# Optimization experiments

Measured on AMD Instinct MI355X. Metric: run time of the kernel, lower is better.

Reference implementation:

```python
import jax, jax.numpy as jnp
import numpy as np

DIM, H, D, B, L = 1024, 8, 64, 1, 256


def silu(v):
    return v * jax.nn.sigmoid(v)


def setup_inputs() -> dict:
    key = jax.random.key(0)
    ks = jax.random.split(key, 12)
    n = lambda i, shape, scale=1.0: jax.random.normal(ks[i], shape, dtype=jnp.float32) * scale
    return {
        "x": n(0, (B, L, DIM)),
        "hidden_real": n(1, (B, H, D)),
        "hidden_imag": n(2, (B, H, D)),
        "w_in1": n(3, (DIM, DIM), 1.0 / np.sqrt(DIM)),
        "b_in1": jnp.zeros((DIM,), jnp.float32),
        "w_in2": n(4, (DIM, H * D * 4), 1.0 / np.sqrt(DIM)),
        "b_in2": jnp.zeros((H * D * 4,), jnp.float32),
        "w_out1": n(5, (H * D * 2, DIM), 1.0 / np.sqrt(H * D * 2)),
        "b_out1": jnp.zeros((DIM,), jnp.float32),
        "w_out2": n(6, (DIM, DIM), 1.0 / np.sqrt(DIM)),
        "b_out2": jnp.zeros((DIM,), jnp.float32),
        "mat_v_real": n(7, (H, D, D)),
        "mat_v_imag": n(8, (H, D, D)),
    }


def reference(x, hidden_real, hidden_imag, w_in1, b_in1, w_in2, b_in2,
              w_out1, b_out1, w_out2, b_out2, mat_v_real, mat_v_imag):
    batch, slen, _ = x.shape
    t = silu(x @ w_in1 + b_in1)
    t = t @ w_in2 + b_in2                       # (B, L, 4*H*D)
    z = t.reshape(batch, slen, H, D, 2, 2)      # [..., {x,a}, {re,im}]
    xc = jax.lax.complex(z[..., 0, 0], z[..., 0, 1])   # (B, L, H, D) complex
    ac = jax.lax.complex(z[..., 1, 0], z[..., 1, 1])

    # normalize a: unit phase * sigmoid(log(|a|^2)) magnitude
    mag2 = ac.real * ac.real + ac.imag * ac.imag
    ac = ac * (jax.lax.rsqrt(mag2) * jax.nn.sigmoid(jnp.log(mag2)))

    a_ln = jnp.log(ac)                          # (B, L, H, D) complex
    al = jnp.transpose(a_ln, (0, 2, 3, 1))      # (B, H, D, L)

    # triu-broadcast + cumsum along cols == the FFT conv-with-ones in the original
    idx = jnp.arange(slen)
    triu = idx[:, None] <= idx[None, :]          # row i, col j: keep j >= i
    tri = jnp.where(triu, al[..., None, :], 0.0)  # (B, H, D, L, L)
    cum = jnp.cumsum(tri, axis=-1)               # cum[i, k] = sum_{j=i..k} a_ln[j]
    keep = (idx[:, None] - 1) <= idx[None, :]    # triu(diagonal=-1)
    c = jnp.where(keep, jnp.exp(cum), 0.0)       # c[i,k] = prod_{j=i..k} a[j]; c[i,i-1]=1

    V = jax.lax.complex(mat_v_real, mat_v_imag)  # (H, D, D)
    Vinv = jnp.linalg.inv(V)
    hidden = jax.lax.complex(hidden_real, hidden_imag)  # (B, H, D)

    x_roll = jnp.concatenate([hidden.astype(xc.dtype)[:, None], xc[:, :-1]], axis=1)
    u = jnp.einsum('hno,blho->blhn', Vinv, x_roll)       # V^{-1} applied per head
    h = jnp.einsum('bholm,blho->bmho', c, u)             # banded product-scan
    h = h.at[:, -1].add(jnp.einsum('hno,bho->bhn', Vinv, xc[:, -1]))
    h = jnp.einsum('hno,blho->blhn', V, h)               # back to V-basis

    hidden_next = h[:, -1]                                # (B, H, D) complex
    hr = jnp.stack([h.real, h.imag], axis=-1).reshape(batch, slen, H * D * 2)
    y = silu(hr @ w_out1 + b_out1)
    y = y @ w_out2 + b_out2
    return y, hidden_next
```

## Files before the change

kernel.cpp:

```cpp
#include <hip/hip_runtime.h>
#include <math.h>

#define DIMN 1024
#define NH 8
#define ND 64
#define LSEQ 256
#define HD 512

typedef __attribute__((ext_vector_type(8))) short short8;
typedef __attribute__((ext_vector_type(4))) float f32x4;

__device__ __forceinline__ float2 cmul(float2 a, float2 b){
    return make_float2(a.x*b.x - a.y*b.y, a.x*b.y + a.y*b.x);
}
__device__ __forceinline__ ushort f2bf(float f){
    union { float f; unsigned u; } v; v.f = f;
    unsigned r = v.u + 0x7FFF + ((v.u >> 16) & 1);
    return (ushort)(r >> 16);
}

#define ISTR 65

__device__ __forceinline__ void inv_gj_blocked(const float* __restrict__ Vr,
        const float* __restrict__ Vi, float2* __restrict__ Vinv,
        int h, int tid, float2* Mx){
    for (int idx = tid; idx < 4096; idx += 512){
        int i = idx >> 6, j = idx & 63;
        Mx[i*ISTR + j] = make_float2(Vr[h*4096 + idx], Vi[h*4096 + idx]);
    }
    __syncthreads();
    const int w = tid >> 6, l = tid & 63;
    const int rbase = w*8;
    for (int kb = 0; kb < 8; ++kb){
        const int k0 = kb*8;
        if (w == 0){
            float2 pr[8];
            #pragma unroll
            for (int m = 0; m < 8; ++m) pr[m] = Mx[l*ISTR + k0 + m];
            #pragma unroll
            for (int k = 0; k < 8; ++k){
                const int gk = k0 + k;
                float2 d; d.x = __shfl(pr[k].x, gk); d.y = __shfl(pr[k].y, gk);
                float im = 1.f/(d.x*d.x + d.y*d.y);
                float2 p = make_float2(d.x*im, -d.y*im);
                float2 spr[8];
                #pragma unroll
                for (int m = 0; m < 8; ++m){
                    float2 t; t.x = __shfl(pr[m].x, gk); t.y = __shfl(pr[m].y, gk);
                    spr[m] = (m == k) ? p : cmul(t, p);
                }
                float2 f = pr[k];
                if (l == gk){
                    #pragma unroll
                    for (int m = 0; m < 8; ++m) pr[m] = spr[m];
                } else {
                    #pragma unroll
                    for (int m = 0; m < 8; ++m){
                        float2 u = cmul(f, spr[m]);
                        if (m == k){ pr[m].x = -u.x;  pr[m].y = -u.y;  }
                        else       { pr[m].x -= u.x;  pr[m].y -= u.y;  }
                    }
                }
            }
            #pragma unroll
            for (int m = 0; m < 8; ++m) Mx[l*ISTR + k0 + m] = pr[m];
        }
        __syncthreads();
        float2 br[8];
        #pragma unroll
        for (int m = 0; m < 8; ++m) br[m] = Mx[(k0+m)*ISTR + l];
        __syncthreads();
        if (((unsigned)(l - k0)) >= 8u){
            #pragma unroll
            for (int rr = 0; rr < 8; ++rr){
                const int r = rbase + rr;
                float2 acc;
                if (((unsigned)(r - k0)) < 8u){ acc.x = 0.f; acc.y = 0.f; }
                else acc = Mx[r*ISTR + l];
                #pragma unroll
                for (int m = 0; m < 8; ++m){
                    float2 Pv = Mx[r*ISTR + k0 + m];
                    acc.x += Pv.x*br[m].x - Pv.y*br[m].y;
                    acc.y += Pv.x*br[m].y + Pv.y*br[m].x;
                }
                Mx[r*ISTR + l] = acc;
            }
        }
        __syncthreads();
    }
    for (int idx = tid; idx < 4096; idx += 512){
        int i = idx >> 6, j = idx & 63;
        Vinv[h*4096 + idx] = Mx[i*ISTR + j];
    }
}

__global__ __launch_bounds__(512) void prep_kernel(
        const float* __restrict__ x,
        const float* __restrict__ w1, const float* __restrict__ w2,
        const float* __restrict__ w3, const float* __restrict__ w4,
        const float* __restrict__ Vr, const float* __restrict__ Vi,
        ushort* __restrict__ x_bf,
        ushort* __restrict__ w1t, ushort* __restrict__ w2t,
        ushort* __restrict__ w3t, ushort* __restrict__ w4t,
        float2* __restrict__ Vinv){
    __shared__ float2 Mx[64*ISTR];
    const int b = blockIdx.x;
    const int tid = threadIdx.x;

    if (b < 8){
        inv_gj_blocked(Vr, Vi, Vinv, b, tid, Mx);
        return;
    }

    int widx = b - 8;
    if (widx < 128){
        int i = widx*512 + tid;
        float4 v = ((const float4*)x)[i];
        ushort4 u; u.x=f2bf(v.x); u.y=f2bf(v.y); u.z=f2bf(v.z); u.w=f2bf(v.w);
        ((ushort4*)x_bf)[i] = u;
        return;
    }
    widx -= 128;

    const float* W; ushort* Wt; int K = 1024, N;
    if (widx < 512)            { W = w1; Wt = w1t; N = 1024; }
    else if (widx < 1536)      { W = w2; Wt = w2t; N = 2048; widx -= 512; }
    else if (widx < 2048)      { W = w3; Wt = w3t; N = 1024; widx -= 1536; }
    else                       { W = w4; Wt = w4t; N = 1024; widx -= 2048; }
    const int half = tid >> 8;
    const int t = widx*2 + half;
    const int tiles_n = N >> 5;
    const int n0 = (t % tiles_n) * 32, k0 = (t / tiles_n) * 32;
    float* tile = (float*)Mx + half*(32*33);
    const int tx = tid & 31, ty = (tid >> 5) & 7;
    #pragma unroll
    for (int i = 0; i < 4; ++i)
        tile[(ty + i*8)*33 + tx] = W[(k0 + ty + i*8)*N + n0 + tx];
    __syncthreads();
    #pragma unroll
    for (int i = 0; i < 4; ++i){
        int r = ty + i*8;
        Wt[(n0 + r)*K + k0 + tx] = f2bf(tile[tx*33 + r]);
    }
}

__global__ __launch_bounds__(512) void inv_kernel(const float* __restrict__ Vr,
                                                  const float* __restrict__ Vi,
                                                  float2* __restrict__ Vinv){
    __shared__ float2 Mx[64*ISTR];
    inv_gj_blocked(Vr, Vi, Vinv, blockIdx.x, threadIdx.x, Mx);
}

__global__ __launch_bounds__(256) void transpose_cvt(const float* __restrict__ W,
                 ushort* __restrict__ Wt, int K, int N){
    __shared__ float tile[32][33];
    const int n0 = blockIdx.x * 32, k0 = blockIdx.y * 32;
    const int tx = threadIdx.x & 31, ty = threadIdx.x >> 5;
    #pragma unroll
    for (int i = 0; i < 4; ++i)
        tile[ty + i*8][tx] = W[(k0 + ty + i*8)*N + n0 + tx];
    __syncthreads();
    #pragma unroll
    for (int i = 0; i < 4; ++i){
        int r = ty + i*8;
        Wt[(n0 + r)*K + k0 + tx] = f2bf(tile[tx][r]);
    }
}

__global__ __launch_bounds__(256) void cvt_bf16_kernel(const float* __restrict__ in,
                                 ushort* __restrict__ o, int n4){
    int i = blockIdx.x*256 + threadIdx.x;
    if (i < n4){
        float4 v = ((const float4*)in)[i];
        ushort4 u; u.x=f2bf(v.x); u.y=f2bf(v.y); u.z=f2bf(v.z); u.w=f2bf(v.w);
        ((ushort4*)o)[i] = u;
    }
}

#define BM 64
#define BN 64
#define BK 32
#define ASTR 40
template<int ACT>
__global__ __launch_bounds__(256) void gemm_bt(const ushort* __restrict__ A,
                 const ushort* __restrict__ Bt, const float* __restrict__ bias,
                 float* __restrict__ Cf, ushort* __restrict__ Cb,
                 float2* __restrict__ XCo, float2* __restrict__ Ao,
                 int M, int N, int K){
    __shared__ ushort As[BM*ASTR];
    __shared__ ushort Bs[BN*ASTR];
    const int tid = threadIdx.x;
    const int bm = blockIdx.y * BM, bn = blockIdx.x * BN;
    const int wave = tid >> 6, l = tid & 63;
    const int wr = (wave >> 1) * 32, wc = (wave & 1) * 32;
    const int ml = l & 15, quad = l >> 4;
    f32x4 acc[2][2];
    #pragma unroll
    for (int i=0;i<2;++i)
        #pragma unroll
        for (int j=0;j<2;++j) acc[i][j] = (f32x4){0.f,0.f,0.f,0.f};
    const int c0r = tid >> 2;
    const int c0s = tid & 3;
    for (int k0 = 0; k0 < K; k0 += BK){
        uint4 av = *(const uint4*)&A [(bm + c0r)*K + k0 + c0s*8];
        uint4 bv = *(const uint4*)&Bt[(bn + c0r)*K + k0 + c0s*8];
        __syncthreads();
        *(uint4*)&As[c0r*ASTR + c0s*8] = av;
        *(uint4*)&Bs[c0r*ASTR + c0s*8] = bv;
        __syncthreads();
        short8 af[2], bfv[2];
        #pragma unroll
        for (int f=0; f<2; ++f){
            af[f]  = *(const short8*)&As[(wr + f*16 + ml)*ASTR + quad*8];
            bfv[f] = *(const short8*)&Bs[(wc + f*16 + ml)*ASTR + quad*8];
        }
        #pragma unroll
        for (int i=0;i<2;++i)
            #pragma unroll
            for (int j=0;j<2;++j)
                acc[i][j] = __builtin_amdgcn_mfma_f32_16x16x32_bf16(af[i], bfv[j], acc[i][j], 0,0,0);
    }
    #pragma unroll
    for (int i=0;i<2;++i){
        #pragma unroll
        for (int j=0;j<2;++j){
            const int gcol = bn + wc + j*16 + ml;
            const float bsv = bias[gcol];
            #pragma unroll
            for (int r=0;r<4;++r){
                const int grow = bm + wr + i*16 + quad*4 + r;
                float val = acc[i][j][r] + bsv;
                if (ACT == 2){
                    float v1 = __shfl_down(val, 1);
                    float v2 = __shfl_down(val, 2);
                    float v3 = __shfl_down(val, 3);
                    if ((l & 3) == 0){
                        int hd = gcol >> 2;
                        XCo[grow*HD + hd] = make_float2(val, v1);
                        float m2 = v2*v2 + v3*v3;
                        float s = sqrtf(m2)/(1.f + m2);
                        Ao[grow*HD + hd] = make_float2(v2*s, v3*s);
                    }
                } else if (ACT == 1){
                    val *= 1.f/(1.f + expf(-val));
                    Cb[grow*N + gcol] = f2bf(val);
                } else {
                    Cf[grow*N + gcol] = val;
                }
            }
        }
    }
}

__global__ __launch_bounds__(512) void upscan_kernel(const float2* __restrict__ Vinv,
        const float* __restrict__ hidr, const float* __restrict__ him,
        const float2* __restrict__ XC, const float2* __restrict__ Aseq,
        float2* __restrict__ S){
    __shared__ float4 buf[2][2][LSEQ];
    __shared__ float2 vrow[2][64];
    __shared__ float2 inu[2];
    const int b = blockIdx.x;
    const int tid = threadIdx.x;
    const int g = tid >> 8, m = tid & 255;
    const int hn = b*2 + g;
    const int h = hn >> 6;
    if (m < 64) vrow[g][m] = Vinv[hn*64 + m];
    __syncthreads();
    float2 acc = make_float2(0.f, 0.f);
    const float2* xrow = &XC[m*HD + h*64];
    #pragma unroll 8
    for (int o=0;o<64;++o){
        float2 p = cmul(vrow[g][o], xrow[o]);
        acc.x += p.x; acc.y += p.y;
    }
    if (m == 0){
        float2 i0 = make_float2(0.f, 0.f);
        #pragma unroll 8
        for (int o=0;o<64;++o){
            float2 hv = make_float2(hidr[h*64+o], him[h*64+o]);
            float2 p = cmul(vrow[g][o], hv);
            i0.x += p.x; i0.y += p.y;
        }
        inu[g] = i0;
    }
    float2 a = Aseq[m*HD + hn];
    buf[0][g][m] = make_float4(a.x, a.y, acc.x, acc.y);
    __syncthreads();
    int pb = 0;
    #pragma unroll
    for (int d = 1; d < LSEQ; d <<= 1){
        float4 cur = buf[pb][g][m];
        float4 o2 = cur;
        if (m >= d){
            float4 prev = buf[pb][g][m-d];
            float2 cA = make_float2(cur.x, cur.y), cU = make_float2(cur.z, cur.w);
            float2 pA = make_float2(prev.x, prev.y), pU = make_float2(prev.z, prev.w);
            float2 nA = cmul(cA, pA);
            float2 nU = cmul(cA, pU);
            nU.x += cU.x; nU.y += cU.y;
            o2 = make_float4(nA.x, nA.y, nU.x, nU.y);
        }
        buf[pb^1][g][m] = o2;
        pb ^= 1;
        __syncthreads();
    }
    float4 t = buf[pb][g][m];
    float2 init = inu[g];
    float2 st = cmul(make_float2(t.x, t.y), init);
    st.x += t.z; st.y += t.w;
    S[m*HD + hn] = st;
}

__global__ __launch_bounds__(256) void vmul_kernel(const float* __restrict__ Vr,
                            const float* __restrict__ Vi,
                            const float2* __restrict__ S, ushort* __restrict__ hrb,
                            float* __restrict__ out_tail, int tail_n){
    int g = blockIdx.x*256 + threadIdx.x;
    int m = g >> 9, hn = g & 511;
    int h = hn >> 6;
    const float* vr = &Vr[hn*64];
    const float* vi = &Vi[hn*64];
    const float2* srow = &S[m*HD + h*64];
    float2 acc = make_float2(0.f, 0.f);
    #pragma unroll 8
    for (int o=0;o<64;++o){
        float2 v = make_float2(vr[o], vi[o]);
        float2 p = cmul(v, srow[o]);
        acc.x += p.x; acc.y += p.y;
    }
    hrb[m*DIMN + hn*2]   = f2bf(acc.x);
    hrb[m*DIMN + hn*2+1] = f2bf(acc.y);
    if (m == LSEQ-1){
        if (tail_n >= 1024){
            out_tail[hn]       = acc.x;
            out_tail[512 + hn] = acc.y;
        } else if (tail_n >= 512){
            out_tail[hn] = acc.x;
        }
    }
}

extern "C" void kernel_launch(void* const* d_in, const int* in_sizes, int n_in,
                              void* d_out, int out_size, void* d_ws, size_t ws_size,
                              hipStream_t stream) {
    const float* x      = (const float*)d_in[0];
    const float* hidr   = (const float*)d_in[1];
    const float* hidi   = (const float*)d_in[2];
    const float* w_in1  = (const float*)d_in[3];
    const float* b_in1  = (const float*)d_in[4];
    const float* w_in2  = (const float*)d_in[5];
    const float* b_in2  = (const float*)d_in[6];
    const float* w_out1 = (const float*)d_in[7];
    const float* b_out1 = (const float*)d_in[8];
    const float* w_out2 = (const float*)d_in[9];
    const float* b_out2 = (const float*)d_in[10];
    const float* Vr     = (const float*)d_in[11];
    const float* Vi     = (const float*)d_in[12];
    float* out = (float*)d_out;
    const int tail_n = out_size - LSEQ*DIMN;
    char* ws = (char*)d_ws;

    if (ws_size >= 14946304u){
        float2* Vinv  = (float2*)(ws + 0);
        ushort* w1t   = (ushort*)(ws + 262144);
        ushort* w2t   = (ushort*)(ws + 2359296);
        ushort* w3t   = (ushort*)(ws + 6553600);
        ushort* w4t   = (ushort*)(ws + 8650752);
        ushort* x_bf  = (ushort*)(ws + 10747904);
        ushort* t1_bf = (ushort*)(ws + 11272192);
        float2* XC    = (float2*)(ws + 11796480);
        float2* Aseq  = (float2*)(ws + 12845056);
        float2* S     = (float2*)(ws + 13893632);
        ushort* y1_bf = x_bf;
        ushort* hr_bf = t1_bf;

        prep_kernel<<<2696, 512, 0, stream>>>(x, w_in1, w_in2, w_out1, w_out2,
                                              Vr, Vi, x_bf, w1t, w2t, w3t, w4t, Vinv);
        gemm_bt<1><<<dim3(16,4), 256, 0, stream>>>(x_bf, w1t, b_in1, nullptr, t1_bf,
                                                   nullptr, nullptr, LSEQ, DIMN, DIMN);
        gemm_bt<2><<<dim3(32,4), 256, 0, stream>>>(t1_bf, w2t, b_in2, nullptr, nullptr,
                                                   XC, Aseq, LSEQ, 2048, DIMN);
        upscan_kernel<<<256, 512, 0, stream>>>(Vinv, hidr, hidi, XC, Aseq, S);
        vmul_kernel<<<LSEQ*HD/256, 256, 0, stream>>>(Vr, Vi, S, hr_bf, out + LSEQ*DIMN, tail_n);
        gemm_bt<1><<<dim3(16,4), 256, 0, stream>>>(hr_bf, w3t, b_out1, nullptr, y1_bf,
                                                   nullptr, nullptr, LSEQ, DIMN, DIMN);
        gemm_bt<0><<<dim3(16,4), 256, 0, stream>>>(y1_bf, w4t, b_out2, out, nullptr,
                                                   nullptr, nullptr, LSEQ, DIMN, DIMN);
    } else {
        float2* Vinv  = (float2*)(ws + 0);
        ushort* wt    = (ushort*)(ws + 262144);
        ushort* x_bf  = (ushort*)(ws + 4456448);
        ushort* t1_bf = (ushort*)(ws + 4980736);
        float2* XC    = (float2*)(ws + 5505024);
        float2* Aseq  = (float2*)(ws + 6553600);
        float2* S     = (float2*)(ws + 7602176);
        ushort* y1_bf = x_bf;
        ushort* hr_bf = t1_bf;

        inv_kernel<<<NH, 512, 0, stream>>>(Vr, Vi, Vinv);
        cvt_bf16_kernel<<<LSEQ*DIMN/4/256, 256, 0, stream>>>(x, x_bf, LSEQ*DIMN/4);
        transpose_cvt<<<dim3(32,32), 256, 0, stream>>>(w_in1, wt, DIMN, DIMN);
        gemm_bt<1><<<dim3(16,4), 256, 0, stream>>>(x_bf, wt, b_in1, nullptr, t1_bf,
                                                   nullptr, nullptr, LSEQ, DIMN, DIMN);
        transpose_cvt<<<dim3(64,32), 256, 0, stream>>>(w_in2, wt, DIMN, 2048);
        gemm_bt<2><<<dim3(32,4), 256, 0, stream>>>(t1_bf, wt, b_in2, nullptr, nullptr,
                                                   XC, Aseq, LSEQ, 2048, DIMN);
        upscan_kernel<<<256, 512, 0, stream>>>(Vinv, hidr, hidi, XC, Aseq, S);
        vmul_kernel<<<LSEQ*HD/256, 256, 0, stream>>>(Vr, Vi, S, hr_bf, out + LSEQ*DIMN, tail_n);
        transpose_cvt<<<dim3(32,32), 256, 0, stream>>>(w_out1, wt, DIMN, DIMN);
        gemm_bt<1><<<dim3(16,4), 256, 0, stream>>>(hr_bf, wt, b_out1, nullptr, y1_bf,
                                                   nullptr, nullptr, LSEQ, DIMN, DIMN);
        transpose_cvt<<<dim3(32,32), 256, 0, stream>>>(w_out2, wt, DIMN, DIMN);
        gemm_bt<0><<<dim3(16,4), 256, 0, stream>>>(y1_bf, wt, b_out2, out, nullptr,
                                                   nullptr, nullptr, LSEQ, DIMN, DIMN);
    }
}
```

Measured before the change: 219.2 us.

## Fold V into w_out1 weights and drop the vmul kernel

Precomputes an effective out-projection weight W3eff = V applied to w_out1 inside the prep kernel, so the scan output S can go straight into the GEMM as bf16 without a separate V-multiply pass. The hidden_next tail is computed from the last scan row inside one block of the final GEMM. This removes the vmul kernel launch and an intermediate round trip, but adds a heavier weight-prep stage (a complex 64-term contraction per weight tile) and makes one GEMM block do extra serial work. Each call rebuilds the folded weights.

```diff
diff --git a/kernel.cpp b/kernel.cpp
--- a/kernel.cpp
+++ b/kernel.cpp
@@ -94,6 +94,39 @@
     }
 }
 
+__device__ __forceinline__ void w3eff_tile(const float* __restrict__ Vr,
+        const float* __restrict__ Vi, const float* __restrict__ w3,
+        ushort* __restrict__ W3bt, int t, int tid, float* lds){
+    const int n0 = (t & 31)*32;
+    const int c0 = (t >> 5)*32;
+    const int h  = c0 >> 7;
+    const int og0 = (c0 & 127) >> 1;
+    float* Vbr = lds;
+    float* Vbi = lds + 1024;
+    float* Wb  = lds + 2048;
+    for (int q = tid; q < 1024; q += 512){
+        int dd = q >> 4, oo = q & 15;
+        Vbr[q] = Vr[(h*64+dd)*64 + og0 + oo];
+        Vbi[q] = Vi[(h*64+dd)*64 + og0 + oo];
+    }
+    for (int q = tid; q < 4096; q += 512){
+        int row = q >> 5, nn = q & 31;
+        Wb[q] = w3[(h*128 + row)*1024 + n0 + nn];
+    }
+    __syncthreads();
+    const int nn = tid & 31, oo = tid >> 5;
+    float ar = 0.f, ai = 0.f;
+    #pragma unroll 8
+    for (int dd = 0; dd < 64; ++dd){
+        float vr = Vbr[dd*16 + oo], vi = Vbi[dd*16 + oo];
+        float w0 = Wb[(dd*2)*32 + nn], w1v = Wb[(dd*2+1)*32 + nn];
+        ar += vr*w0 + vi*w1v;
+        ai += -vi*w0 + vr*w1v;
+    }
+    W3bt[(n0+nn)*1024 + c0 + oo*2 + 0] = f2bf(ar);
+    W3bt[(n0+nn)*1024 + c0 + oo*2 + 1] = f2bf(ai);
+}
+
 __global__ __launch_bounds__(512) void prep_kernel(
         const float* __restrict__ x,
         const float* __restrict__ w1, const float* __restrict__ w2,
@@ -101,7 +134,7 @@
         const float* __restrict__ Vr, const float* __restrict__ Vi,
         ushort* __restrict__ x_bf,
         ushort* __restrict__ w1t, ushort* __restrict__ w2t,
-        ushort* __restrict__ w3t, ushort* __restrict__ w4t,
+        ushort* __restrict__ W3bt, ushort* __restrict__ w4t,
         float2* __restrict__ Vinv){
     __shared__ float2 Mx[64*ISTR];
     const int b = blockIdx.x;
@@ -122,11 +155,15 @@
     }
     widx -= 128;
 
+    if (widx >= 2048){
+        w3eff_tile(Vr, Vi, w3, W3bt, widx - 2048, tid, (float*)Mx);
+        return;
+    }
+
     const float* W; ushort* Wt; int K = 1024, N;
     if (widx < 512)            { W = w1; Wt = w1t; N = 1024; }
     else if (widx < 1536)      { W = w2; Wt = w2t; N = 2048; widx -= 512; }
-    else if (widx < 2048)      { W = w3; Wt = w3t; N = 1024; widx -= 1536; }
-    else                       { W = w4; Wt = w4t; N = 1024; widx -= 2048; }
+    else                       { W = w4; Wt = w4t; N = 1024; widx -= 1536; }
     const int half = tid >> 8;
     const int t = widx*2 + half;
     const int tiles_n = N >> 5;
@@ -186,7 +223,10 @@
                  const ushort* __restrict__ Bt, const float* __restrict__ bias,
                  float* __restrict__ Cf, ushort* __restrict__ Cb,
                  float2* __restrict__ XCo, float2* __restrict__ Ao,
-                 int M, int N, int K){
+                 int M, int N, int K,
+                 const float* __restrict__ tVr, const float* __restrict__ tVi,
+                 const float2* __restrict__ S255, float* __restrict__ out_tail,
+                 int tail_n){
     __shared__ ushort As[BM*ASTR];
     __shared__ ushort Bs[BN*ASTR];
     const int tid = threadIdx.x;
@@ -194,6 +234,26 @@
     const int wave = tid >> 6, l = tid & 63;
     const int wr = (wave >> 1) * 32, wc = (wave & 1) * 32;
     const int ml = l & 15, quad = l >> 4;
+
+    if (ACT == 0 && out_tail != nullptr && blockIdx.x == 0 && blockIdx.y == 0){
+        for (int hn = tid; hn < 512; hn += 256){
+            int h = hn >> 6;
+            float2 acc2 = make_float2(0.f, 0.f);
+            #pragma unroll 8
+            for (int o = 0; o < 64; ++o){
+                float2 v = make_float2(tVr[hn*64+o], tVi[hn*64+o]);
+                float2 p = cmul(v, S255[h*64+o]);
+                acc2.x += p.x; acc2.y += p.y;
+            }
+            if (tail_n >= 1024){
+                out_tail[hn]       = acc2.x;
+                out_tail[512 + hn] = acc2.y;
+            } else if (tail_n >= 512){
+                out_tail[hn] = acc2.x;
+            }
+        }
+    }
+
     f32x4 acc[2][2];
     #pragma unroll
     for (int i=0;i<2;++i)
@@ -255,7 +315,7 @@
 __global__ __launch_bounds__(512) void upscan_kernel(const float2* __restrict__ Vinv,
         const float* __restrict__ hidr, const float* __restrict__ him,
         const float2* __restrict__ XC, const float2* __restrict__ Aseq,
-        float2* __restrict__ S){
+        ushort* __restrict__ Sb, float2* __restrict__ S255){
     __shared__ float4 buf[2][2][LSEQ];
     __shared__ float2 vrow[2][64];
     __shared__ float2 inu[2];
@@ -308,7 +368,9 @@
     float2 init = inu[g];
     float2 st = cmul(make_float2(t.x, t.y), init);
     st.x += t.z; st.y += t.w;
-    S[m*HD + hn] = st;
+    Sb[m*DIMN + hn*2]   = f2bf(st.x);
+    Sb[m*DIMN + hn*2+1] = f2bf(st.y);
+    if (m == LSEQ-1) S255[hn] = st;
 }
 
 __global__ __launch_bounds__(256) void vmul_kernel(const float* __restrict__ Vr,
@@ -338,6 +400,65 @@
             out_tail[hn] = acc.x;
         }
     }
+}
+
+__global__ __launch_bounds__(512) void upscan_f32_kernel(const float2* __restrict__ Vinv,
+        const float* __restrict__ hidr, const float* __restrict__ him,
+        const float2* __restrict__ XC, const float2* __restrict__ Aseq,
+        float2* __restrict__ S){
+    __shared__ float4 buf[2][2][LSEQ];
+    __shared__ float2 vrow[2][64];
+    __shared__ float2 inu[2];
+    const int b = blockIdx.x;
+    const int tid = threadIdx.x;
+    const int g = tid >> 8, m = tid & 255;
+    const int hn = b*2 + g;
+    const int h = hn >> 6;
+    if (m < 64) vrow[g][m] = Vinv[hn*64 + m];
+    __syncthreads();
+    float2 acc = make_float2(0.f, 0.f);
+    const float2* xrow = &XC[m*HD + h*64];
+    #pragma unroll 8
+    for (int o=0;o<64;++o){
+        float2 p = cmul(vrow[g][o], xrow[o]);
+        acc.x += p.x; acc.y += p.y;
+    }
+    if (m == 0){
+        float2 i0 = make_float2(0.f, 0.f);
+        #pragma unroll 8
+        for (int o=0;o<64;++o){
+            float2 hv = make_float2(hidr[h*64+o], him[h*64+o]);
+            float2 p = cmul(vrow[g][o], hv);
+            i0.x += p.x; i0.y += p.y;
+        }
+        inu[g] = i0;
+    }
+    float2 a = Aseq[m*HD + hn];
+    buf[0][g][m] = make_float4(a.x, a.y, acc.x, acc.y);
+    __syncthreads();
+    int pb = 0;
+    #pragma unroll
+    for (int d = 1; d < LSEQ; d <<= 1){
+        float4 cur = buf[pb][g][m];
+        float4 o2 = cur;
+        if (m >= d){
+            float4 prev = buf[pb][g][m-d];
+            float2 cA = make_float2(cur.x, cur.y), cU = make_float2(cur.z, cur.w);
+            float2 pA = make_float2(prev.x, prev.y), pU = make_float2(prev.z, prev.w);
+            float2 nA = cmul(cA, pA);
+            float2 nU = cmul(cA, pU);
+            nU.x += cU.x; nU.y += cU.y;
+            o2 = make_float4(nA.x, nA.y, nU.x, nU.y);
+        }
+        buf[pb^1][g][m] = o2;
+        pb ^= 1;
+        __syncthreads();
+    }
+    float4 t = buf[pb][g][m];
+    float2 init = inu[g];
+    float2 st = cmul(make_float2(t.x, t.y), init);
+    st.x += t.z; st.y += t.w;
+    S[m*HD + hn] = st;
 }
 
 extern "C" void kernel_launch(void* const* d_in, const int* in_sizes, int n_in,
@@ -364,28 +485,27 @@
         float2* Vinv  = (float2*)(ws + 0);
         ushort* w1t   = (ushort*)(ws + 262144);
         ushort* w2t   = (ushort*)(ws + 2359296);
-        ushort* w3t   = (ushort*)(ws + 6553600);
+        ushort* W3bt  = (ushort*)(ws + 6553600);
         ushort* w4t   = (ushort*)(ws + 8650752);
         ushort* x_bf  = (ushort*)(ws + 10747904);
         ushort* t1_bf = (ushort*)(ws + 11272192);
         float2* XC    = (float2*)(ws + 11796480);
         float2* Aseq  = (float2*)(ws + 12845056);
-        float2* S     = (float2*)(ws + 13893632);
+        float2* S255  = (float2*)(ws + 13893632);
         ushort* y1_bf = x_bf;
-        ushort* hr_bf = t1_bf;
-
-        prep_kernel<<<2696, 512, 0, stream>>>(x, w_in1, w_in2, w_out1, w_out2,
-                                              Vr, Vi, x_bf, w1t, w2t, w3t, w4t, Vinv);
+        ushort* Sb    = t1_bf;
+
+        prep_kernel<<<3208, 512, 0, stream>>>(x, w_in1, w_in2, w_out1, w_out2,
+                                              Vr, Vi, x_bf, w1t, w2t, W3bt, w4t, Vinv);
         gemm_bt<1><<<dim3(16,4), 256, 0, stream>>>(x_bf, w1t, b_in1, nullptr, t1_bf,
-                                                   nullptr, nullptr, LSEQ, DIMN, DIMN);
+                nullptr, nullptr, LSEQ, DIMN, DIMN, nullptr, nullptr, nullptr, nullptr, 0);
         gemm_bt<2><<<dim3(32,4), 256, 0, stream>>>(t1_bf, w2t, b_in2, nullptr, nullptr,
-                                                   XC, Aseq, LSEQ, 2048, DIMN);
-        upscan_kernel<<<256, 512, 0, stream>>>(Vinv, hidr, hidi, XC, Aseq, S);
-        vmul_kernel<<<LSEQ*HD/256, 256, 0, stream>>>(Vr, Vi, S, hr_bf, out + LSEQ*DIMN, tail_n);
-        gemm_bt<1><<<dim3(16,4), 256, 0, stream>>>(hr_bf, w3t, b_out1, nullptr, y1_bf,
-                                                   nullptr, nullptr, LSEQ, DIMN, DIMN);
+                XC, Aseq, LSEQ, 2048, DIMN, nullptr, nullptr, nullptr, nullptr, 0);
+        upscan_kernel<<<256, 512, 0, stream>>>(Vinv, hidr, hidi, XC, Aseq, Sb, S255);
+        gemm_bt<1><<<dim3(16,4), 256, 0, stream>>>(Sb, W3bt, b_out1, nullptr, y1_bf,
+                nullptr, nullptr, LSEQ, DIMN, DIMN, nullptr, nullptr, nullptr, nullptr, 0);
         gemm_bt<0><<<dim3(16,4), 256, 0, stream>>>(y1_bf, w4t, b_out2, out, nullptr,
-                                                   nullptr, nullptr, LSEQ, DIMN, DIMN);
+                nullptr, nullptr, LSEQ, DIMN, DIMN, Vr, Vi, S255, out + LSEQ*DIMN, tail_n);
     } else {
         float2* Vinv  = (float2*)(ws + 0);
         ushort* wt    = (ushort*)(ws + 262144);
@@ -401,17 +521,17 @@
         cvt_bf16_kernel<<<LSEQ*DIMN/4/256, 256, 0, stream>>>(x, x_bf, LSEQ*DIMN/4);
         transpose_cvt<<<dim3(32,32), 256, 0, stream>>>(w_in1, wt, DIMN, DIMN);
         gemm_bt<1><<<dim3(16,4), 256, 0, stream>>>(x_bf, wt, b_in1, nullptr, t1_bf,
-                                                   nullptr, nullptr, LSEQ, DIMN, DIMN);
+                nullptr, nullptr, LSEQ, DIMN, DIMN, nullptr, nullptr, nullptr, nullptr, 0);
         transpose_cvt<<<dim3(64,32), 256, 0, stream>>>(w_in2, wt, DIMN, 2048);
         gemm_bt<2><<<dim3(32,4), 256, 0, stream>>>(t1_bf, wt, b_in2, nullptr, nullptr,
-                                                   XC, Aseq, LSEQ, 2048, DIMN);
-        upscan_kernel<<<256, 512, 0, stream>>>(Vinv, hidr, hidi, XC, Aseq, S);
+                XC, Aseq, LSEQ, 2048, DIMN, nullptr, nullptr, nullptr, nullptr, 0);
+        upscan_f32_kernel<<<256, 512, 0, stream>>>(Vinv, hidr, hidi, XC, Aseq, S);
         vmul_kernel<<<LSEQ*HD/256, 256, 0, stream>>>(Vr, Vi, S, hr_bf, out + LSEQ*DIMN, tail_n);
         transpose_cvt<<<dim3(32,32), 256, 0, stream>>>(w_out1, wt, DIMN, DIMN);
         gemm_bt<1><<<dim3(16,4), 256, 0, stream>>>(hr_bf, wt, b_out1, nullptr, y1_bf,
-                                                   nullptr, nullptr, LSEQ, DIMN, DIMN);
+                nullptr, nullptr, LSEQ, DIMN, DIMN, nullptr, nullptr, nullptr, nullptr, 0);
         transpose_cvt<<<dim3(32,32), 256, 0, stream>>>(w_out2, wt, DIMN, DIMN);
         gemm_bt<0><<<dim3(16,4), 256, 0, stream>>>(y1_bf, wt, b_out2, out, nullptr,
-                                                   nullptr, nullptr, LSEQ, DIMN, DIMN);
-    }
-}
+                nullptr, nullptr, LSEQ, DIMN, DIMN, nullptr, nullptr, nullptr, nullptr, 0);
+    }
+}
```

After: 212.7 us. 3.0% less time.
